# Kernel optimization log

Hardware: AMD Instinct MI355X
Metric: run time of the kernel (lower is better)

## Reference

```python
import jax, jax.numpy as jnp
import numpy as np

B, N, L, D, H, GOUT = 256, 307, 12, 16, 8, 32


def pos_encoding():
    # positional_encoding(X, 16): P[1, L, D]
    pos = jnp.arange(L, dtype=jnp.float32)[:, None]
    div = jnp.power(10000.0, jnp.arange(0, D, 2, dtype=jnp.float32) / D)
    ang = pos / div  # [L, D/2]
    P = jnp.zeros((L, D), dtype=jnp.float32)
    P = P.at[:, 0::2].set(jnp.sin(ang)).at[:, 1::2].set(jnp.cos(ang))
    return P[None]  # [1, L, D]


def setup_inputs() -> dict:
    key = jax.random.key(0)
    ks = jax.random.split(key, 24)
    s = 0.02
    inp = {
        "flow_x": jax.random.normal(ks[0], (B, N, L), dtype=jnp.float32),
        "day_cyc": jax.random.randint(ks[1], (B, L), 0, 289),
        "week_cyc": jax.random.randint(ks[2], (B, L), 0, 8),
        "adj": (jax.random.uniform(ks[3], (N, N)) < 0.03).astype(jnp.float32),
        "day_emb": jax.random.normal(ks[4], (289, D), dtype=jnp.float32) * s,
        "week_emb": jax.random.normal(ks[5], (8, D), dtype=jnp.float32) * s,
        "Wq": jax.random.normal(ks[6], (D, D), dtype=jnp.float32) * s,
        "bq": jnp.zeros((D,), jnp.float32),
        "Wk": jax.random.normal(ks[7], (D, D), dtype=jnp.float32) * s,
        "bk": jnp.zeros((D,), jnp.float32),
        "Wv": jax.random.normal(ks[8], (D, D), dtype=jnp.float32) * s,
        "bv": jnp.zeros((D,), jnp.float32),
        "Wo": jax.random.normal(ks[9], (D, D), dtype=jnp.float32) * s,
        "bo": jnp.zeros((D,), jnp.float32),
        "Wg": jax.random.normal(ks[10], (1, GOUT), dtype=jnp.float32) * s,
        "Wt": jax.random.normal(ks[11], (D, GOUT), dtype=jnp.float32) * s,
        "bg": jnp.zeros((GOUT,), jnp.float32),
        "W1": jax.random.normal(ks[12], (N, GOUT, 8), dtype=jnp.float32) * s,
        "b1": jnp.zeros((N, 8), jnp.float32),
        "W2": jax.random.normal(ks[13], (N, 8, 1), dtype=jnp.float32) * s,
        "b2": jnp.zeros((N, 1), jnp.float32),
    }
    return inp


def dyn_graph(flow_x):
    # his_win[:, 0:12] = flow_x[0]; his_win[:, 11+b] = flow_x[b, :, -1] for b>=1
    his = jnp.concatenate([flow_x[0], flow_x[1:, :, -1].T], axis=1)  # [N, 11+B]
    sq = jnp.sum(his * his, axis=1)
    d2 = sq[:, None] + sq[None, :] - 2.0 * (his @ his.T)
    return jnp.sqrt(jnp.maximum(d2, 0.0))  # [N, N] euclidean distances


def reference(flow_x, day_cyc, week_cyc, adj, day_emb, week_emb,
              Wq, bq, Wk, bk, Wv, bv, Wo, bo, Wg, Wt, bg, W1, b1, W2, b2):
    hd = D // H  # head dim = 2
    fun_graph = dyn_graph(flow_x)                          # [N, N]
    pe = pos_encoding()                                    # [1, L, D]
    te = day_emb[day_cyc] + week_emb[week_cyc]             # [B, L, D]
    x_t = flow_x[..., None] + pe[:, None] + te[:, None]    # [B, N, L, D]

    # multi-head self-attention over time axis (8 heads, dim 16)
    def heads(x, W, b):
        return (x @ W + b).reshape(x.shape[0], x.shape[1], L, H, hd)
    q, k, v = heads(x_t, Wq, bq), heads(x_t, Wk, bk), heads(x_t, Wv, bv)
    logits = jnp.einsum('bnlhd,bnmhd->bnhlm', q, k) / jnp.sqrt(jnp.float32(hd))
    att = jnp.einsum('bnhlm,bnmhd->bnlhd', jax.nn.softmax(logits, axis=-1), v)
    att = att.reshape(flow_x.shape[0], N, L, D) @ Wo + bo
    x_tcn = x_t + att                                      # [B, N, L, D]

    # graph-temporal block: dynamic-graph message passing + static-graph mix
    A_dyn = jax.nn.softmax(-fun_graph, axis=-1)            # closer vertices weigh more
    A_st = adj / (jnp.sum(adj, axis=-1, keepdims=True) + 1.0)
    x_gcn = flow_x[..., None]                              # [B, N, L, 1]
    hid = jax.nn.relu(
        jnp.einsum('nm,bmlc->bnlc', A_dyn, x_gcn @ Wg)
        + jnp.einsum('nm,bmlc->bnlc', A_st, x_tcn @ Wt)
        + bg)                                              # [B, N, L, 32]

    # per-vertex 2-layer MLPs, batched over N (replaces the Python loop)
    h1 = jax.nn.relu(jnp.einsum('bnlc,nco->bnlo', hid, W1) + b1[None, :, None])
    out = jnp.einsum('bnlo,noz->bnlz', h1, W2) + b2[None, :, None]
    return out[..., 0]                                     # [B, N, 12]
```

## Files before the change

kernel.cpp:

```cpp
#include <hip/hip_runtime.h>
#include <hip/hip_bf16.h>
#include <math.h>

#define NB 256
#define NN 307
#define NBN 78592
#define LL 12
#define DDIM 16
#define HISW 268
#define HIS4 67
#define NBRCAP 64
#define AGRP 32
#define ADTS 308

#define OFF_XTCN 0u
#define OFF_TEK  7544832u
#define OFF_G1   15089664u
#define OFF_ADT  16032768u
#define OFF_TEQ  16127456u
#define OFF_HIS  16176608u
#define OFF_NW   16258896u
#define OFF_NIDX 16278544u
#define OFF_NCNT 16298192u
#define OFF_TEV  16298512u
#define OFF_TEO  16347664u

__device__ inline float4 mkf4(float a, float b, float c, float d) {
    float4 r; r.x = a; r.y = b; r.z = c; r.w = d; return r;
}
__device__ inline float bf_lo(unsigned u) { return __uint_as_float(u << 16); }
__device__ inline float bf_hi(unsigned u) { return __uint_as_float(u & 0xffff0000u); }

__global__ __launch_bounds__(256) void prep_kernel(
    const float* __restrict__ flow,
    const int* __restrict__ dayc, const int* __restrict__ weekc,
    const float* __restrict__ demb, const float* __restrict__ wemb,
    const float* __restrict__ Wq, const float* __restrict__ bq,
    const float* __restrict__ Wk, const float* __restrict__ bk,
    const float* __restrict__ Wv, const float* __restrict__ bv,
    const float* __restrict__ bo, const float* __restrict__ adj,
    float* __restrict__ his,
    float* __restrict__ TEQ, float* __restrict__ TEK,
    float* __restrict__ TEV, float* __restrict__ TEO,
    int* __restrict__ ncnt, int* __restrict__ nidx, float* __restrict__ nw) {
    __shared__ float sTE[16][16];
    int bx = blockIdx.x, t = threadIdx.x;
    if (bx < 322) {
        int e = bx * 256 + t;
        if (e < NN * HISW) {
            int n = e / HISW, j = e - n * HISW;
            float v = 0.f;
            if (j < LL) v = flow[n * LL + j];
            else if (j < 267) v = flow[((j - 11) * NN + n) * LL + 11];
            his[e] = v;
        }
    } else if (bx < 514) {
        int r = t >> 4, d = t & 15;
        int row = (bx - 322) * 16 + r;
        int b = row / LL, l = row - b * LL;
        int dc = dayc[b * LL + l], wc = weekc[b * LL + l];
        int i = d >> 1;
        float ang = (float)l * powf(10000.f, -0.125f * (float)i);
        float pe = (d & 1) ? cosf(ang) : sinf(ang);
        float te = demb[dc * DDIM + d] + wemb[wc * DDIM + d] + pe;
        sTE[r][d] = te;
        __syncthreads();
        float aq = bq[d], ak = bk[d], av = bv[d];
#pragma unroll
        for (int e = 0; e < 16; e++) {
            float x = sTE[r][e];
            aq += x * Wq[e * 16 + d];
            ak += x * Wk[e * 16 + d];
            av += x * Wv[e * 16 + d];
        }
        TEQ[row * 16 + d] = aq * 0.70710678118654752f;
        TEK[row * 16 + d] = ak;
        TEV[row * 16 + d] = av;
        TEO[row * 16 + d] = te + bo[d];
    } else {
        if (t < 64) {
            int n = bx - 514;
            float rs = 0.f;
            for (int m0 = 0; m0 < NN; m0 += 64) {
                int m = m0 + t;
                if (m < NN) rs += adj[n * NN + m];
            }
            for (int off = 32; off > 0; off >>= 1) rs += __shfl_xor(rs, off);
            float inv = 1.f / (rs + 1.f);
            int c = 0;
            for (int m0 = 0; m0 < NN; m0 += 64) {
                int m = m0 + t;
                float a = (m < NN) ? adj[n * NN + m] : 0.f;
                bool p = (a != 0.f);
                unsigned long long mask = __ballot(p);
                int pos = __popcll(mask & ((1ull << t) - 1ull));
                if (p && (c + pos) < NBRCAP) {
                    nidx[n * NBRCAP + c + pos] = m;
                    nw[n * NBRCAP + c + pos] = a * inv;
                }
                c += (int)__popcll(mask);
            }
            if (t == 0) ncnt[n] = c < NBRCAP ? c : NBRCAP;
        }
    }
}

__global__ __launch_bounds__(256) void adyn_kernel(const float* __restrict__ his,
                                                   float* __restrict__ AdT) {
    __shared__ float4 sh[HIS4];
    __shared__ float red[256];
    int n = blockIdx.x, t = threadIdx.x;
    if (t < HIS4) sh[t] = reinterpret_cast<const float4*>(his)[n * HIS4 + t];
    __syncthreads();

    float e0 = 0.f, e1 = 0.f, lsum = 0.f;
    {
        const float4* row = reinterpret_cast<const float4*>(his) + t * HIS4;
        float4 acc = mkf4(0.f, 0.f, 0.f, 0.f);
        for (int j = 0; j < HIS4; j++) {
            float4 a = sh[j], b = row[j];
            float dx = a.x - b.x, dy = a.y - b.y, dz = a.z - b.z, dw = a.w - b.w;
            acc.x += dx * dx; acc.y += dy * dy; acc.z += dz * dz; acc.w += dw * dw;
        }
        float d2 = (acc.x + acc.y) + (acc.z + acc.w);
        e0 = __expf(-sqrtf(fmaxf(d2, 0.f)));
        lsum += e0;
    }
    int m1 = t + 256;
    if (m1 < NN) {
        const float4* row = reinterpret_cast<const float4*>(his) + m1 * HIS4;
        float4 acc = mkf4(0.f, 0.f, 0.f, 0.f);
        for (int j = 0; j < HIS4; j++) {
            float4 a = sh[j], b = row[j];
            float dx = a.x - b.x, dy = a.y - b.y, dz = a.z - b.z, dw = a.w - b.w;
            acc.x += dx * dx; acc.y += dy * dy; acc.z += dz * dz; acc.w += dw * dw;
        }
        float d2 = (acc.x + acc.y) + (acc.z + acc.w);
        e1 = __expf(-sqrtf(fmaxf(d2, 0.f)));
        lsum += e1;
    }
    red[t] = lsum;
    __syncthreads();
    for (int s = 128; s > 0; s >>= 1) {
        if (t < s) red[t] += red[t + s];
        __syncthreads();
    }
    float inv = 1.f / red[0];
    AdT[t * ADTS + n] = e0 * inv;
    if (m1 < NN) AdT[m1 * ADTS + n] = e1 * inv;
}

__global__ __launch_bounds__(256) void attn_kernel(
    const float* __restrict__ flow,
    const float* __restrict__ TEQ, const float* __restrict__ TEK,
    const float* __restrict__ TEV, const float* __restrict__ TEO,
    const float* __restrict__ Wq, const float* __restrict__ Wk,
    const float* __restrict__ Wv, const float* __restrict__ Wo,
    unsigned short* __restrict__ xtcn) {
    __shared__ __align__(16) float sWo[256];
    __shared__ __align__(16) float sWs[48];
    __shared__ __align__(16) float sT[4][24][16];
    __shared__ __align__(16) float sA[AGRP][LL][20];

    const int t = threadIdx.x;
    const int bn0 = blockIdx.x * AGRP;
    const int b0 = bn0 / NN;
    const int rbase = b0 * LL;

    sWo[t] = Wo[t];
    if (t < 48) {
        int mat = t >> 4, d = t & 15;
        const float* W = (mat == 0) ? Wq : (mat == 1) ? Wk : Wv;
        float s = 0.f;
#pragma unroll
        for (int e = 0; e < 16; e++) s += W[e * 16 + d];
        sWs[t] = (mat == 0) ? s * 0.70710678118654752f : s;
    }
#pragma unroll
    for (int p = 0; p < 2; p++) {
        int idx = t + p * 256;
        if (idx < 384) {
            int tab = idx / 96, rr4 = idx - tab * 96;
            int rr = rr4 >> 2, j = rr4 & 3;
            int row = rbase + rr;
            if (row < NB * LL) {
                const float* src = (tab == 0) ? TEQ : (tab == 1) ? TEK : (tab == 2) ? TEV : TEO;
                reinterpret_cast<float4*>(&sT[tab][rr][0])[j] =
                    reinterpret_cast<const float4*>(src + row * 16)[j];
            }
        }
    }
    __syncthreads();

    {
        int g = t >> 3, h = t & 7;
        int bn = bn0 + g;
        int b = bn / NN;
        int lb = (b - b0) * LL;
        float f[12];
        {
            const float4* fr = reinterpret_cast<const float4*>(flow + bn * LL);
            float4 f0 = fr[0], f1 = fr[1], f2 = fr[2];
            f[0] = f0.x; f[1] = f0.y; f[2] = f0.z; f[3] = f0.w;
            f[4] = f1.x; f[5] = f1.y; f[6] = f1.z; f[7] = f1.w;
            f[8] = f2.x; f[9] = f2.y; f[10] = f2.z; f[11] = f2.w;
        }
        float wqx = sWs[2 * h], wqy = sWs[2 * h + 1];
        float wkx = sWs[16 + 2 * h], wky = sWs[16 + 2 * h + 1];
        float wvx = sWs[32 + 2 * h], wvy = sWs[32 + 2 * h + 1];
        float kx[12], ky[12], vx[12], vy[12];
#pragma unroll
        for (int m = 0; m < LL; m++) {
            float2 tk = *reinterpret_cast<const float2*>(&sT[1][lb + m][2 * h]);
            float2 tv = *reinterpret_cast<const float2*>(&sT[2][lb + m][2 * h]);
            kx[m] = tk.x + f[m] * wkx; ky[m] = tk.y + f[m] * wky;
            vx[m] = tv.x + f[m] * wvx; vy[m] = tv.y + f[m] * wvy;
        }
#pragma unroll
        for (int l = 0; l < LL; l++) {
            float2 tq = *reinterpret_cast<const float2*>(&sT[0][lb + l][2 * h]);
            float qx = tq.x + f[l] * wqx, qy = tq.y + f[l] * wqy;
            float s[12];
            float sum = 0.f;
#pragma unroll
            for (int m = 0; m < LL; m++) {
                s[m] = __expf(qx * kx[m] + qy * ky[m]);
                sum += s[m];
            }
            float a0 = 0.f, a1 = 0.f;
#pragma unroll
            for (int m = 0; m < LL; m++) { a0 += s[m] * vx[m]; a1 += s[m] * vy[m]; }
            float inv = 1.f / sum;
            float2 r; r.x = a0 * inv; r.y = a1 * inv;
            *reinterpret_cast<float2*>(&sA[g][l][2 * h]) = r;
        }
    }
    __syncthreads();

#pragma unroll
    for (int p = 0; p < 2; p++) {
        int jb = t + p * 256;
        if (jb < AGRP * LL) {
            int g = jb / LL, l = jb - g * LL;
            int bn = bn0 + g;
            int b = bn / NN;
            int lb = (b - b0) * LL;
            float f = flow[bn * LL + l];
            float att[16];
            const float4* ar = reinterpret_cast<const float4*>(&sA[g][l][0]);
            float4 a0 = ar[0], a1 = ar[1], a2 = ar[2], a3 = ar[3];
            att[0] = a0.x; att[1] = a0.y; att[2] = a0.z; att[3] = a0.w;
            att[4] = a1.x; att[5] = a1.y; att[6] = a1.z; att[7] = a1.w;
            att[8] = a2.x; att[9] = a2.y; att[10] = a2.z; att[11] = a2.w;
            att[12] = a3.x; att[13] = a3.y; att[14] = a3.z; att[15] = a3.w;
            float o[16];
            const float4* to4 = reinterpret_cast<const float4*>(&sT[3][lb + l][0]);
#pragma unroll
            for (int j = 0; j < 4; j++) {
                float4 a = to4[j];
                o[4 * j] = a.x; o[4 * j + 1] = a.y; o[4 * j + 2] = a.z; o[4 * j + 3] = a.w;
            }
#pragma unroll
            for (int e = 0; e < 16; e++) {
                float ae = att[e];
                const float4* wo = reinterpret_cast<const float4*>(&sWo[e * 16]);
#pragma unroll
                for (int j = 0; j < 4; j++) {
                    float4 w = wo[j];
                    o[4 * j] += ae * w.x; o[4 * j + 1] += ae * w.y;
                    o[4 * j + 2] += ae * w.z; o[4 * j + 3] += ae * w.w;
                }
            }
            unsigned pk[8];
#pragma unroll
            for (int j = 0; j < 8; j++) {
                unsigned u0 = __float_as_uint(o[2 * j] + f) + 0x8000u;
                unsigned u1 = __float_as_uint(o[2 * j + 1] + f) + 0x8000u;
                pk[j] = (u0 >> 16) | (u1 & 0xffff0000u);
            }
            uint4* dst = reinterpret_cast<uint4*>(xtcn + (size_t)bn * 192 + l * 16);
            uint4 d0; d0.x = pk[0]; d0.y = pk[1]; d0.z = pk[2]; d0.w = pk[3];
            uint4 d1; d1.x = pk[4]; d1.y = pk[5]; d1.z = pk[6]; d1.w = pk[7];
            dst[0] = d0; dst[1] = d1;
        }
    }
}

__global__ __launch_bounds__(256) void g1_kernel(const float* __restrict__ flow,
                                                 const float* __restrict__ AdT,
                                                 float* __restrict__ G1) {
    int bp = blockIdx.x, nt = blockIdx.y, t = threadIdx.x;
    int lane = t & 63;
    int l0 = (t >> 6) * 3;
    int l0u = __builtin_amdgcn_readfirstlane(l0);
    int n = nt * 128 + 2 * lane;
    int b0 = 2 * bp;
    const float* fb0 = flow + (size_t)b0 * (NN * LL);
    const float* fb1 = fb0 + NN * LL;

    float a000 = 0.f, a001 = 0.f, a002 = 0.f;
    float a010 = 0.f, a011 = 0.f, a012 = 0.f;
    float a100 = 0.f, a101 = 0.f, a102 = 0.f;
    float a110 = 0.f, a111 = 0.f, a112 = 0.f;
#pragma unroll 4
    for (int m = 0; m < NN; m++) {
        float2 w = reinterpret_cast<const float2*>(AdT + (size_t)m * ADTS + nt * 128)[lane];
        const float* r0 = fb0 + m * LL + l0u;
        const float* r1 = fb1 + m * LL + l0u;
        float p0 = r0[0], p1 = r0[1], p2 = r0[2];
        float q0 = r1[0], q1 = r1[1], q2 = r1[2];
        a000 += w.x * p0; a001 += w.x * p1; a002 += w.x * p2;
        a010 += w.y * p0; a011 += w.y * p1; a012 += w.y * p2;
        a100 += w.x * q0; a101 += w.x * q1; a102 += w.x * q2;
        a110 += w.y * q0; a111 += w.y * q1; a112 += w.y * q2;
    }
    if (n < NN) {
        float* d0 = G1 + ((size_t)b0 * NN + n) * LL + l0;
        d0[0] = a000; d0[1] = a001; d0[2] = a002;
        float* d1 = G1 + ((size_t)(b0 + 1) * NN + n) * LL + l0;
        d1[0] = a100; d1[1] = a101; d1[2] = a102;
    }
    if (n + 1 < NN) {
        float* d0 = G1 + ((size_t)b0 * NN + n + 1) * LL + l0;
        d0[0] = a010; d0[1] = a011; d0[2] = a012;
        float* d1 = G1 + ((size_t)(b0 + 1) * NN + n + 1) * LL + l0;
        d1[0] = a110; d1[1] = a111; d1[2] = a112;
    }
}

__global__ __launch_bounds__(256) void final_kernel(
    const unsigned short* __restrict__ xtcn, const float* __restrict__ G1,
    const float* __restrict__ Wg, const float* __restrict__ Wt,
    const float* __restrict__ bg, const float* __restrict__ W1,
    const float* __restrict__ b1, const float* __restrict__ W2,
    const float* __restrict__ b2, const int* __restrict__ ncnt,
    const int* __restrict__ nidx, const float* __restrict__ nw,
    float* __restrict__ out) {
    __shared__ __align__(16) float sWt[512];
    __shared__ __align__(16) float sW1[256];
    __shared__ __align__(16) float sWg[32];
    __shared__ __align__(16) float sBg[32];
    __shared__ float sB1[8], sW2[8];
    __shared__ __align__(16) float sY[4][240];
    __shared__ __align__(16) float4 sHID[4][120];
    __shared__ float sH1[4][96];

    int t = threadIdx.x;
    int by = blockIdx.x;
    int n  = blockIdx.y;
    int w = t >> 6, t64 = t & 63;
    int b = by * 4 + w;

    sW1[t] = W1[n * 256 + t];
    sWt[t] = Wt[t];
    sWt[t + 256] = Wt[t + 256];
    if (t < 32) sWg[t] = Wg[t];
    else if (t < 64) sBg[t - 32] = bg[t - 32];
    else if (t < 72) sB1[t - 64] = b1[n * 8 + (t - 64)];
    else if (t < 80) sW2[t - 72] = W2[n * 8 + (t - 72)];
    float vb2 = b2[n];
    int cnt = ncnt[n];
    __syncthreads();

    if (t64 < 48) {
        float y0 = 0.f, y1 = 0.f, y2 = 0.f, y3 = 0.f;
        const unsigned short* base = xtcn + (size_t)b * NN * 192;
        int i = 0;
        for (; i + 3 < cnt; i += 4) {
            int m0 = nidx[n * NBRCAP + i],     m1 = nidx[n * NBRCAP + i + 1];
            int m2 = nidx[n * NBRCAP + i + 2], m3 = nidx[n * NBRCAP + i + 3];
            float w0 = nw[n * NBRCAP + i],     w1 = nw[n * NBRCAP + i + 1];
            float w2 = nw[n * NBRCAP + i + 2], w3 = nw[n * NBRCAP + i + 3];
            uint2 p0 = reinterpret_cast<const uint2*>(base + m0 * 192)[t64];
            uint2 p1 = reinterpret_cast<const uint2*>(base + m1 * 192)[t64];
            uint2 p2 = reinterpret_cast<const uint2*>(base + m2 * 192)[t64];
            uint2 p3 = reinterpret_cast<const uint2*>(base + m3 * 192)[t64];
            y0 += w0 * bf_lo(p0.x) + w1 * bf_lo(p1.x) + w2 * bf_lo(p2.x) + w3 * bf_lo(p3.x);
            y1 += w0 * bf_hi(p0.x) + w1 * bf_hi(p1.x) + w2 * bf_hi(p2.x) + w3 * bf_hi(p3.x);
            y2 += w0 * bf_lo(p0.y) + w1 * bf_lo(p1.y) + w2 * bf_lo(p2.y) + w3 * bf_lo(p3.y);
            y3 += w0 * bf_hi(p0.y) + w1 * bf_hi(p1.y) + w2 * bf_hi(p2.y) + w3 * bf_hi(p3.y);
        }
        for (; i < cnt; i++) {
            int ma = nidx[n * NBRCAP + i];
            float wa = nw[n * NBRCAP + i];
            uint2 pa = reinterpret_cast<const uint2*>(base + ma * 192)[t64];
            y0 += wa * bf_lo(pa.x); y1 += wa * bf_hi(pa.x);
            y2 += wa * bf_lo(pa.y); y3 += wa * bf_hi(pa.y);
        }
        int l = t64 >> 2, p = t64 & 3;
        reinterpret_cast<float4*>(&sY[w][l * 20])[p] = mkf4(y0, y1, y2, y3);
    }
    __syncthreads();

#pragma unroll
    for (int p = 0; p < 2; p++) {
        int jb = t + p * 256;
        if (jb < 384) {
            int w2 = jb / 96, c = jb - w2 * 96;
            int b2i = by * 4 + w2;
            int l = c >> 3, j = c & 7;
            float g = G1[((size_t)b2i * NN + n) * LL + l];
            float4 wg = reinterpret_cast<const float4*>(sWg)[j];
            float4 acc = reinterpret_cast<const float4*>(sBg)[j];
            acc.x += g * wg.x; acc.y += g * wg.y; acc.z += g * wg.z; acc.w += g * wg.w;
            const float4* yr = reinterpret_cast<const float4*>(&sY[w2][l * 20]);
            float4 v0 = yr[0], v1 = yr[1], v2 = yr[2], v3 = yr[3];
            float ye[16] = {v0.x, v0.y, v0.z, v0.w, v1.x, v1.y, v1.z, v1.w,
                            v2.x, v2.y, v2.z, v2.w, v3.x, v3.y, v3.z, v3.w};
#pragma unroll
            for (int d = 0; d < 16; d++) {
                float4 wt = reinterpret_cast<const float4*>(sWt)[d * 8 + j];
                acc.x += ye[d] * wt.x; acc.y += ye[d] * wt.y;
                acc.z += ye[d] * wt.z; acc.w += ye[d] * wt.w;
            }
            acc.x = fmaxf(acc.x, 0.f); acc.y = fmaxf(acc.y, 0.f);
            acc.z = fmaxf(acc.z, 0.f); acc.w = fmaxf(acc.w, 0.f);
            sHID[w2][l * 10 + j] = acc;
        }
    }
    __syncthreads();

#pragma unroll
    for (int p = 0; p < 2; p++) {
        int jb = t + p * 256;
        if (jb < 384) {
            int w2 = jb / 96, o = jb - w2 * 96;
            int l = o >> 3, oo = o & 7;
            float acc = sB1[oo];
            float he[32];
#pragma unroll
            for (int k = 0; k < 8; k++) {
                float4 hv = sHID[w2][l * 10 + k];
                he[4 * k + 0] = hv.x; he[4 * k + 1] = hv.y;
                he[4 * k + 2] = hv.z; he[4 * k + 3] = hv.w;
            }
#pragma unroll
            for (int c = 0; c < 32; c++) acc += he[c] * sW1[c * 8 + oo];
            sH1[w2][o] = fmaxf(acc, 0.f);
        }
    }
    __syncthreads();

    if (t < 48) {
        int w2 = t / 12, l = t - w2 * 12;
        const float4* h4 = reinterpret_cast<const float4*>(&sH1[w2][l * 8]);
        float4 ha = h4[0], hb = h4[1];
        const float4* w4 = reinterpret_cast<const float4*>(sW2);
        float4 wa = w4[0], wb = w4[1];
        float acc = vb2 + ha.x * wa.x + ha.y * wa.y + ha.z * wa.z + ha.w * wa.w
                        + hb.x * wb.x + hb.y * wb.y + hb.z * wb.z + hb.w * wb.w;
        out[((size_t)(by * 4 + w2) * NN + n) * LL + l] = acc;
    }
}

extern "C" void kernel_launch(void* const* d_in, const int* in_sizes, int n_in,
                              void* d_out, int out_size, void* d_ws, size_t ws_size,
                              hipStream_t stream) {
    const float* flow = (const float*)d_in[0];
    const int* dayc   = (const int*)d_in[1];
    const int* weekc  = (const int*)d_in[2];
    const float* adj  = (const float*)d_in[3];
    const float* demb = (const float*)d_in[4];
    const float* wemb = (const float*)d_in[5];
    const float* Wq = (const float*)d_in[6];  const float* bq = (const float*)d_in[7];
    const float* Wk = (const float*)d_in[8];  const float* bk = (const float*)d_in[9];
    const float* Wv = (const float*)d_in[10]; const float* bv = (const float*)d_in[11];
    const float* Wo = (const float*)d_in[12]; const float* bo = (const float*)d_in[13];
    const float* Wg = (const float*)d_in[14]; const float* Wt = (const float*)d_in[15];
    const float* bg = (const float*)d_in[16];
    const float* W1 = (const float*)d_in[17]; const float* b1 = (const float*)d_in[18];
    const float* W2 = (const float*)d_in[19]; const float* b2 = (const float*)d_in[20];
    float* out = (float*)d_out;
    float* ws  = (float*)d_ws;

    unsigned short* xtcn = (unsigned short*)(ws + 0);
    float* TEK  = ws + OFF_TEK;
    float* G1   = ws + OFF_G1;
    float* AdT  = ws + OFF_ADT;
    float* TEQ  = ws + OFF_TEQ;
    float* TEV  = ws + OFF_TEV;
    float* TEO  = ws + OFF_TEO;
    float* his  = ws + OFF_HIS;
    float* nw   = ws + OFF_NW;
    int*   nidx = (int*)(ws + OFF_NIDX);
    int*   ncnt = (int*)(ws + OFF_NCNT);

    prep_kernel<<<821, 256, 0, stream>>>(flow, dayc, weekc, demb, wemb,
                                         Wq, bq, Wk, bk, Wv, bv, bo, adj,
                                         his, TEQ, TEK, TEV, TEO, ncnt, nidx, nw);
    adyn_kernel<<<NN, 256, 0, stream>>>(his, AdT);
    attn_kernel<<<NBN / AGRP, 256, 0, stream>>>(flow, TEQ, TEK, TEV, TEO,
                                                Wq, Wk, Wv, Wo, xtcn);
    g1_kernel<<<dim3(NB / 2, 3), 256, 0, stream>>>(flow, AdT, G1);
    final_kernel<<<dim3(64, NN), 256, 0, stream>>>(xtcn, G1, Wg, Wt, bg, W1, b1, W2, b2,
                                                   ncnt, nidx, nw, out);
}
```

Baseline: 263.5 us.

## Restructure final kernel to one thread per (batch, time) with register-resident MLP

The final kernel now assigns each thread one (batch, time step) pair. It gathers the full 16-wide neighbour-weighted sum in registers, then computes the 32-channel hidden layer and both MLP layers without intermediate shared-memory stages or extra barriers. Neighbour indices and weights are staged in shared memory, Wt is stored transposed, and each block covers 16 batches with 192 threads, which cuts the grid to a quarter. The cost is higher register pressure (y[16], h1[8]), fewer blocks, and per-thread 32-byte gathers that are less coalesced across a wave.

```diff
diff --git a/kernel.cpp b/kernel.cpp
--- a/kernel.cpp
+++ b/kernel.cpp
@@ -328,7 +328,7 @@
     }
 }
 
-__global__ __launch_bounds__(256) void final_kernel(
+__global__ __launch_bounds__(192) void final_kernel(
     const unsigned short* __restrict__ xtcn, const float* __restrict__ G1,
     const float* __restrict__ Wg, const float* __restrict__ Wt,
     const float* __restrict__ bg, const float* __restrict__ W1,
@@ -336,121 +336,93 @@
     const float* __restrict__ b2, const int* __restrict__ ncnt,
     const int* __restrict__ nidx, const float* __restrict__ nw,
     float* __restrict__ out) {
-    __shared__ __align__(16) float sWt[512];
+    __shared__ __align__(16) float sWtT[512];
     __shared__ __align__(16) float sW1[256];
     __shared__ __align__(16) float sWg[32];
     __shared__ __align__(16) float sBg[32];
-    __shared__ float sB1[8], sW2[8];
-    __shared__ __align__(16) float sY[4][240];
-    __shared__ __align__(16) float4 sHID[4][120];
-    __shared__ float sH1[4][96];
-
-    int t = threadIdx.x;
-    int by = blockIdx.x;
-    int n  = blockIdx.y;
-    int w = t >> 6, t64 = t & 63;
-    int b = by * 4 + w;
-
+    __shared__ __align__(16) float sB1[8];
+    __shared__ __align__(16) float sW2[8];
+    __shared__ __align__(16) float sNw[64];
+    __shared__ int sNidx[64];
+
+    const int t = threadIdx.x;
+    const int bx = blockIdx.x;
+    const int n  = blockIdx.y;
+    const int b16 = t / LL, l = t - b16 * LL;
+    const int b = bx * 16 + b16;
+
+    const float g = G1[((size_t)b * NN + n) * LL + l];
+    const float vb2 = b2[n];
+    const int cnt = ncnt[n];
+
+    sWtT[t]       = Wt[(t & 15) * 32 + (t >> 4)];
+    { int i2 = t + 192; sWtT[i2] = Wt[(i2 & 15) * 32 + (i2 >> 4)]; }
+    if (t < 128) { int i3 = t + 384; sWtT[i3] = Wt[(i3 & 15) * 32 + (i3 >> 4)]; }
     sW1[t] = W1[n * 256 + t];
-    sWt[t] = Wt[t];
-    sWt[t + 256] = Wt[t + 256];
-    if (t < 32) sWg[t] = Wg[t];
-    else if (t < 64) sBg[t - 32] = bg[t - 32];
-    else if (t < 72) sB1[t - 64] = b1[n * 8 + (t - 64)];
-    else if (t < 80) sW2[t - 72] = W2[n * 8 + (t - 72)];
-    float vb2 = b2[n];
-    int cnt = ncnt[n];
+    if (t < 64) sW1[t + 192] = W1[n * 256 + t + 192];
+    if (t < 64) { sNidx[t] = nidx[n * NBRCAP + t]; sNw[t] = nw[n * NBRCAP + t]; }
+    else if (t < 96)  sWg[t - 64] = Wg[t - 64];
+    else if (t < 128) sBg[t - 96] = bg[t - 96];
+    else if (t < 136) sB1[t - 128] = b1[n * 8 + (t - 128)];
+    else if (t < 144) sW2[t - 136] = W2[n * 8 + (t - 136)];
     __syncthreads();
 
-    if (t64 < 48) {
-        float y0 = 0.f, y1 = 0.f, y2 = 0.f, y3 = 0.f;
-        const unsigned short* base = xtcn + (size_t)b * NN * 192;
-        int i = 0;
-        for (; i + 3 < cnt; i += 4) {
-            int m0 = nidx[n * NBRCAP + i],     m1 = nidx[n * NBRCAP + i + 1];
-            int m2 = nidx[n * NBRCAP + i + 2], m3 = nidx[n * NBRCAP + i + 3];
-            float w0 = nw[n * NBRCAP + i],     w1 = nw[n * NBRCAP + i + 1];
-            float w2 = nw[n * NBRCAP + i + 2], w3 = nw[n * NBRCAP + i + 3];
-            uint2 p0 = reinterpret_cast<const uint2*>(base + m0 * 192)[t64];
-            uint2 p1 = reinterpret_cast<const uint2*>(base + m1 * 192)[t64];
-            uint2 p2 = reinterpret_cast<const uint2*>(base + m2 * 192)[t64];
-            uint2 p3 = reinterpret_cast<const uint2*>(base + m3 * 192)[t64];
-            y0 += w0 * bf_lo(p0.x) + w1 * bf_lo(p1.x) + w2 * bf_lo(p2.x) + w3 * bf_lo(p3.x);
-            y1 += w0 * bf_hi(p0.x) + w1 * bf_hi(p1.x) + w2 * bf_hi(p2.x) + w3 * bf_hi(p3.x);
-            y2 += w0 * bf_lo(p0.y) + w1 * bf_lo(p1.y) + w2 * bf_lo(p2.y) + w3 * bf_lo(p3.y);
-            y3 += w0 * bf_hi(p0.y) + w1 * bf_hi(p1.y) + w2 * bf_hi(p2.y) + w3 * bf_hi(p3.y);
-        }
-        for (; i < cnt; i++) {
-            int ma = nidx[n * NBRCAP + i];
-            float wa = nw[n * NBRCAP + i];
-            uint2 pa = reinterpret_cast<const uint2*>(base + ma * 192)[t64];
-            y0 += wa * bf_lo(pa.x); y1 += wa * bf_hi(pa.x);
-            y2 += wa * bf_lo(pa.y); y3 += wa * bf_hi(pa.y);
-        }
-        int l = t64 >> 2, p = t64 & 3;
-        reinterpret_cast<float4*>(&sY[w][l * 20])[p] = mkf4(y0, y1, y2, y3);
-    }
-    __syncthreads();
-
-#pragma unroll
-    for (int p = 0; p < 2; p++) {
-        int jb = t + p * 256;
-        if (jb < 384) {
-            int w2 = jb / 96, c = jb - w2 * 96;
-            int b2i = by * 4 + w2;
-            int l = c >> 3, j = c & 7;
-            float g = G1[((size_t)b2i * NN + n) * LL + l];
-            float4 wg = reinterpret_cast<const float4*>(sWg)[j];
-            float4 acc = reinterpret_cast<const float4*>(sBg)[j];
-            acc.x += g * wg.x; acc.y += g * wg.y; acc.z += g * wg.z; acc.w += g * wg.w;
-            const float4* yr = reinterpret_cast<const float4*>(&sY[w2][l * 20]);
-            float4 v0 = yr[0], v1 = yr[1], v2 = yr[2], v3 = yr[3];
-            float ye[16] = {v0.x, v0.y, v0.z, v0.w, v1.x, v1.y, v1.z, v1.w,
-                            v2.x, v2.y, v2.z, v2.w, v3.x, v3.y, v3.z, v3.w};
-#pragma unroll
-            for (int d = 0; d < 16; d++) {
-                float4 wt = reinterpret_cast<const float4*>(sWt)[d * 8 + j];
-                acc.x += ye[d] * wt.x; acc.y += ye[d] * wt.y;
-                acc.z += ye[d] * wt.z; acc.w += ye[d] * wt.w;
-            }
-            acc.x = fmaxf(acc.x, 0.f); acc.y = fmaxf(acc.y, 0.f);
-            acc.z = fmaxf(acc.z, 0.f); acc.w = fmaxf(acc.w, 0.f);
-            sHID[w2][l * 10 + j] = acc;
-        }
-    }
-    __syncthreads();
-
-#pragma unroll
-    for (int p = 0; p < 2; p++) {
-        int jb = t + p * 256;
-        if (jb < 384) {
-            int w2 = jb / 96, o = jb - w2 * 96;
-            int l = o >> 3, oo = o & 7;
-            float acc = sB1[oo];
-            float he[32];
-#pragma unroll
-            for (int k = 0; k < 8; k++) {
-                float4 hv = sHID[w2][l * 10 + k];
-                he[4 * k + 0] = hv.x; he[4 * k + 1] = hv.y;
-                he[4 * k + 2] = hv.z; he[4 * k + 3] = hv.w;
-            }
-#pragma unroll
-            for (int c = 0; c < 32; c++) acc += he[c] * sW1[c * 8 + oo];
-            sH1[w2][o] = fmaxf(acc, 0.f);
-        }
-    }
-    __syncthreads();
-
-    if (t < 48) {
-        int w2 = t / 12, l = t - w2 * 12;
-        const float4* h4 = reinterpret_cast<const float4*>(&sH1[w2][l * 8]);
-        float4 ha = h4[0], hb = h4[1];
-        const float4* w4 = reinterpret_cast<const float4*>(sW2);
-        float4 wa = w4[0], wb = w4[1];
-        float acc = vb2 + ha.x * wa.x + ha.y * wa.y + ha.z * wa.z + ha.w * wa.w
-                        + hb.x * wb.x + hb.y * wb.y + hb.z * wb.z + hb.w * wb.w;
-        out[((size_t)(by * 4 + w2) * NN + n) * LL + l] = acc;
-    }
+    float y[16];
+#pragma unroll
+    for (int d = 0; d < 16; d++) y[d] = 0.f;
+    {
+        const unsigned short* bl = xtcn + (size_t)b * (NN * 192) + l * 16;
+        for (int i = 0; i < cnt; i++) {
+            int m = sNidx[i];
+            float w = sNw[i];
+            const uint4* p = reinterpret_cast<const uint4*>(bl + (size_t)m * 192);
+            uint4 u0 = p[0], u1 = p[1];
+            y[0]  += w * bf_lo(u0.x); y[1]  += w * bf_hi(u0.x);
+            y[2]  += w * bf_lo(u0.y); y[3]  += w * bf_hi(u0.y);
+            y[4]  += w * bf_lo(u0.z); y[5]  += w * bf_hi(u0.z);
+            y[6]  += w * bf_lo(u0.w); y[7]  += w * bf_hi(u0.w);
+            y[8]  += w * bf_lo(u1.x); y[9]  += w * bf_hi(u1.x);
+            y[10] += w * bf_lo(u1.y); y[11] += w * bf_hi(u1.y);
+            y[12] += w * bf_lo(u1.z); y[13] += w * bf_hi(u1.z);
+            y[14] += w * bf_lo(u1.w); y[15] += w * bf_hi(u1.w);
+        }
+    }
+
+    float h1[8];
+    {
+        const float4* b14 = reinterpret_cast<const float4*>(sB1);
+        float4 ba = b14[0], bb = b14[1];
+        h1[0] = ba.x; h1[1] = ba.y; h1[2] = ba.z; h1[3] = ba.w;
+        h1[4] = bb.x; h1[5] = bb.y; h1[6] = bb.z; h1[7] = bb.w;
+    }
+#pragma unroll
+    for (int c = 0; c < 32; c++) {
+        const float4* wt = reinterpret_cast<const float4*>(&sWtT[c * 16]);
+        float4 w0 = wt[0], w1 = wt[1], w2 = wt[2], w3 = wt[3];
+        float hc = sBg[c] + g * sWg[c];
+        hc += y[0] * w0.x + y[1] * w0.y + y[2]  * w0.z + y[3]  * w0.w;
+        hc += y[4] * w1.x + y[5] * w1.y + y[6]  * w1.z + y[7]  * w1.w;
+        hc += y[8] * w2.x + y[9] * w2.y + y[10] * w2.z + y[11] * w2.w;
+        hc += y[12] * w3.x + y[13] * w3.y + y[14] * w3.z + y[15] * w3.w;
+        hc = fmaxf(hc, 0.f);
+        const float4* wr = reinterpret_cast<const float4*>(&sW1[c * 8]);
+        float4 a = wr[0], bq4 = wr[1];
+        h1[0] += hc * a.x;   h1[1] += hc * a.y;
+        h1[2] += hc * a.z;   h1[3] += hc * a.w;
+        h1[4] += hc * bq4.x; h1[5] += hc * bq4.y;
+        h1[6] += hc * bq4.z; h1[7] += hc * bq4.w;
+    }
+
+    float acc = vb2;
+    {
+        const float4* w24 = reinterpret_cast<const float4*>(sW2);
+        float4 wa = w24[0], wb = w24[1];
+        acc += fmaxf(h1[0], 0.f) * wa.x + fmaxf(h1[1], 0.f) * wa.y
+             + fmaxf(h1[2], 0.f) * wa.z + fmaxf(h1[3], 0.f) * wa.w
+             + fmaxf(h1[4], 0.f) * wb.x + fmaxf(h1[5], 0.f) * wb.y
+             + fmaxf(h1[6], 0.f) * wb.z + fmaxf(h1[7], 0.f) * wb.w;
+    }
+    out[((size_t)b * NN + n) * LL + l] = acc;
 }
 
 extern "C" void kernel_launch(void* const* d_in, const int* in_sizes, int n_in,
@@ -492,6 +464,6 @@
     attn_kernel<<<NBN / AGRP, 256, 0, stream>>>(flow, TEQ, TEK, TEV, TEO,
                                                 Wq, Wk, Wv, Wo, xtcn);
     g1_kernel<<<dim3(NB / 2, 3), 256, 0, stream>>>(flow, AdT, G1);
-    final_kernel<<<dim3(64, NN), 256, 0, stream>>>(xtcn, G1, Wg, Wt, bg, W1, b1, W2, b2,
+    final_kernel<<<dim3(16, NN), 192, 0, stream>>>(xtcn, G1, Wg, Wt, bg, W1, b1, W2, b2,
                                                    ncnt, nidx, nw, out);
 }
```

Result: faster. 249.4 us (-5.3%).
